# Performance work log

Measured on AMD Instinct MI355X. Metric: run time of the kernel, lower is better.

Reference implementation:

```python
import jax, jax.numpy as jnp
import numpy as np
import math

B, S, H, NH = 2, 2048, 2048, 16
HD = H // NH
BASE = 10000.0


def _rope_tables():
    inv_freq = 1.0 / (BASE ** (np.arange(0, HD, 2, dtype=np.float32) / HD))
    t = np.arange(S, dtype=np.float32)
    freqs = np.einsum('i,j->ij', t, inv_freq)          # [S, HD/2]
    emb = np.concatenate([freqs, freqs], axis=-1)       # [S, HD]
    return jnp.asarray(np.cos(emb)), jnp.asarray(np.sin(emb))


def setup_inputs() -> dict:
    key = jax.random.key(0)
    ks = jax.random.split(key, 6)
    scale = 1.0 / math.sqrt(H)
    cos, sin = _rope_tables()
    causal = np.triu(np.full((S, S), -1e9, dtype=np.float32), k=1)
    attn_bias = jnp.broadcast_to(jnp.asarray(causal)[None, None], (B, 1, S, S))
    return {
        'hidden_states': jax.random.normal(ks[0], (B, S, H), jnp.float32),
        'masks': jnp.zeros((B, S, S), jnp.float32),
        'attn_bias': attn_bias,
        'cos': cos,
        'sin': sin,
        'wq': jax.random.normal(ks[1], (H, H), jnp.float32) * scale,
        'wk': jax.random.normal(ks[2], (H, H), jnp.float32) * scale,
        'wv': jax.random.normal(ks[3], (H, H), jnp.float32) * scale,
        'wo': jax.random.normal(ks[4], (H, H), jnp.float32) * scale,
        'position_ids': jnp.broadcast_to(jnp.arange(S, dtype=jnp.int64)[None], (B, S)),
    }


def _rotate_half(x):
    x1, x2 = x[..., : x.shape[-1] // 2], x[..., x.shape[-1] // 2:]
    return jnp.concatenate([-x2, x1], axis=-1)


def reference(hidden_states, masks, attn_bias, cos, sin, wq, wk, wv, wo, position_ids):
    b, s, h = hidden_states.shape
    nh, hd = NH, HD
    # QKV projections (torch Linear: x @ W.T), split heads -> [b, nh, s, hd]
    def proj(w):
        return (hidden_states @ w.T).reshape(b, s, nh, hd).transpose(0, 2, 1, 3)
    q, k, v = proj(wq), proj(wk), proj(wv)
    # RoPE
    cos_p = cos[position_ids][:, None]  # [b, 1, s, hd]
    sin_p = sin[position_ids][:, None]
    q = q * cos_p + _rotate_half(q) * sin_p
    k = k * cos_p + _rotate_half(k) * sin_p
    # attention scores with additive masks (mx_attn branch, fp math)
    att = jnp.einsum('bhqd,bhkd->bhqk', q / math.sqrt(hd), k)
    att = att + attn_bias + masks[:, None]
    att = jax.nn.softmax(att, axis=-1)
    out = jnp.einsum('bhqk,bhkd->bhqd', att, v)
    out = out.transpose(0, 2, 1, 3).reshape(b, s, h)
    return out @ wo.T
```

## Files before the change

### kernel.cpp

```cpp
#include <hip/hip_runtime.h>
#include <stdint.h>

#define B_  2
#define S_  2048
#define H_  2048
#define NH_ 16
#define HD_ 128

typedef __bf16 v8bf __attribute__((ext_vector_type(8)));
typedef float  v4f  __attribute__((ext_vector_type(4)));

__device__ __forceinline__ float b2f(unsigned short u) {
  union { unsigned int i; float f; } x; x.i = ((unsigned int)u) << 16; return x.f;
}
__device__ __forceinline__ unsigned short f2b(float f) {
  union { float f; unsigned int i; } x; x.f = f;
  unsigned int r = x.i + 0x7FFFu + ((x.i >> 16) & 1u);
  return (unsigned short)(r >> 16);
}

__device__ __forceinline__ void async16(const void* g, void* l) {
  __builtin_amdgcn_global_load_lds(
      (const __attribute__((address_space(1))) void*)g,
      (__attribute__((address_space(3))) void*)l, 16, 0, 0);
}

__global__ __launch_bounds__(256) void cvt_all(const float* __restrict__ hid,
                                               const float* __restrict__ wq,
                                               const float* __restrict__ wk,
                                               const float* __restrict__ wv,
                                               const float* __restrict__ wo,
                                               unsigned short* __restrict__ Xb,
                                               unsigned short* __restrict__ Wqb,
                                               unsigned short* __restrict__ Wkb,
                                               unsigned short* __restrict__ Wvb,
                                               unsigned short* __restrict__ Wob) {
  int bid = blockIdx.x;
  const float* src;
  unsigned short* dst;
  int rel;
  if (bid < 8192)       { src = hid; dst = Xb;  rel = bid; }
  else if (bid < 12288) { src = wq;  dst = Wqb; rel = bid - 8192; }
  else if (bid < 16384) { src = wk;  dst = Wkb; rel = bid - 12288; }
  else if (bid < 20480) { src = wv;  dst = Wvb; rel = bid - 16384; }
  else                  { src = wo;  dst = Wob; rel = bid - 20480; }
  int i = rel * 256 + threadIdx.x;
  float4 f = *(const float4*)(src + (size_t)i * 4);
  ushort4 u;
  u.x = f2b(f.x); u.y = f2b(f.y); u.z = f2b(f.z); u.w = f2b(f.w);
  *(ushort4*)(dst + (size_t)i * 4) = u;
}

__device__ __forceinline__ void gemm_tile_nt(const unsigned short* __restrict__ A,
                                             const unsigned short* __restrict__ Bm,
                                             int m0, int n0, int Kdim,
                                             unsigned short* As, unsigned short* Bs,
                                             v4f (&acc)[2][8]) {
  const int tid = threadIdx.x;
  const int lane = tid & 63, w = tid >> 6;
  const int lr = lane & 15, lg = lane >> 4;
  const int wm = w * 32;

  for (int k0 = 0; k0 < Kdim; k0 += 32) {
    __syncthreads();
#pragma unroll
    for (int i = 0; i < 2; ++i) {
      const int cbase = i * 256 + w * 64;
      const int cc = cbase + lane;
      const int row = cc >> 2, col = (cc & 3) << 3;
      async16(A  + (size_t)(m0 + row) * Kdim + k0 + col, (char*)As + (size_t)cbase * 16);
      async16(Bm + (size_t)(n0 + row) * Kdim + k0 + col, (char*)Bs + (size_t)cbase * 16);
    }
    __syncthreads();
    v8bf a[2], bb[8];
#pragma unroll
    for (int i = 0; i < 2; i++) a[i]  = *(const v8bf*)(As + (wm + i * 16 + lr) * 32 + lg * 8);
#pragma unroll
    for (int i = 0; i < 8; i++) bb[i] = *(const v8bf*)(Bs + (i * 16 + lr) * 32 + lg * 8);
#pragma unroll
    for (int mi = 0; mi < 2; mi++)
#pragma unroll
      for (int ni = 0; ni < 8; ni++)
        acc[mi][ni] = __builtin_amdgcn_mfma_f32_16x16x32_bf16(a[mi], bb[ni], acc[mi][ni], 0, 0, 0);
  }
}

__global__ __launch_bounds__(256, 2) void gemm_qkv(const unsigned short* __restrict__ X,
                                                   const unsigned short* __restrict__ Wq,
                                                   const unsigned short* __restrict__ Wk,
                                                   const unsigned short* __restrict__ Wv,
                                                   const float* __restrict__ cosT,
                                                   const float* __restrict__ sinT,
                                                   unsigned short* __restrict__ Qo,
                                                   unsigned short* __restrict__ Ko,
                                                   unsigned short* __restrict__ Vt) {
  __shared__ unsigned short As[128 * 32], Bs[128 * 32];
  const int m0 = blockIdx.x * 128;
  const int ny = blockIdx.y;
  const int sel = ny >> 4;
  const int h = ny & 15;
  const unsigned short* Bm = (sel == 0) ? Wq : (sel == 1 ? Wk : Wv);
  const int n0 = h * 128;

  v4f acc[2][8];
#pragma unroll
  for (int i = 0; i < 2; i++)
#pragma unroll
    for (int j = 0; j < 8; j++) { v4f z = {0.f, 0.f, 0.f, 0.f}; acc[i][j] = z; }

  gemm_tile_nt(X, Bm, m0, n0, H_, As, Bs, acc);

  const int lane = threadIdx.x & 63, w = threadIdx.x >> 6;
  const int lr = lane & 15, lg = lane >> 4;
  const int rbase = m0 + w * 32;

  if (sel < 2) {
    unsigned short* Out = (sel == 0) ? Qo : Ko;
    const float sc = (sel == 0) ? (float)(0.08838834764831845 * 1.4426950408889634) : 1.0f;
#pragma unroll
    for (int mi = 0; mi < 2; mi++)
#pragma unroll
      for (int ni = 0; ni < 4; ni++)
#pragma unroll
        for (int r = 0; r < 4; r++) {
          int row = rbase + mi * 16 + lg * 4 + r;
          int s = row & 2047;
          int d = ni * 16 + lr;
          float c  = cosT[(size_t)s * HD_ + d];
          float sn = sinT[(size_t)s * HD_ + d];
          float x1 = acc[mi][ni][r], x2 = acc[mi][ni + 4][r];
          Out[(size_t)row * H_ + n0 + d]      = f2b((x1 * c - x2 * sn) * sc);
          Out[(size_t)row * H_ + n0 + d + 64] = f2b((x2 * c + x1 * sn) * sc);
        }
  } else {
#pragma unroll
    for (int mi = 0; mi < 2; mi++)
#pragma unroll
      for (int ni = 0; ni < 8; ni++) {
        int row0 = rbase + mi * 16 + lg * 4;
        int b = row0 >> 11, s0 = row0 & 2047;
        int d = ni * 16 + lr;
        ushort4 u;
        u.x = f2b(acc[mi][ni][0]); u.y = f2b(acc[mi][ni][1]);
        u.z = f2b(acc[mi][ni][2]); u.w = f2b(acc[mi][ni][3]);
        *(ushort4*)(Vt + ((size_t)((b * NH_ + h) * HD_) + d) * S_ + s0) = u;
      }
  }
}

__global__ __launch_bounds__(256, 2) void gemm_out(const unsigned short* __restrict__ A,
                                                   const unsigned short* __restrict__ Wo,
                                                   float* __restrict__ Out) {
  __shared__ unsigned short As[128 * 32], Bs[128 * 32];
  const int m0 = blockIdx.x * 128;
  const int n0 = blockIdx.y * 128;

  v4f acc[2][8];
#pragma unroll
  for (int i = 0; i < 2; i++)
#pragma unroll
    for (int j = 0; j < 8; j++) { v4f z = {0.f, 0.f, 0.f, 0.f}; acc[i][j] = z; }

  gemm_tile_nt(A, Wo, m0, n0, H_, As, Bs, acc);

  const int lane = threadIdx.x & 63, w = threadIdx.x >> 6;
  const int lr = lane & 15, lg = lane >> 4;
#pragma unroll
  for (int mi = 0; mi < 2; mi++)
#pragma unroll
    for (int ni = 0; ni < 8; ni++)
#pragma unroll
      for (int r = 0; r < 4; r++)
        Out[(size_t)(m0 + w * 32 + mi * 16 + lg * 4 + r) * H_ + n0 + ni * 16 + lr] =
            acc[mi][ni][r];
}

#define KT_ 64

__global__ __launch_bounds__(512, 2) void attn_kernel(const unsigned short* __restrict__ Qb,
                                                      const unsigned short* __restrict__ Kb,
                                                      const unsigned short* __restrict__ Vt,
                                                      unsigned short* __restrict__ Ob) {
  __shared__ __align__(16) char smem[90112];
  unsigned short* Ps = (unsigned short*)(smem + 71680);

  const int tid = threadIdx.x, lane = tid & 63, w = tid >> 6;
  const int lr = lane & 15, lg = lane >> 4;
  const int qp = blockIdx.x, h = blockIdx.y, b = blockIdx.z;

  const int wtile = (w < 4) ? qp : (15 - qp);
  const int wrow = wtile * 128 + (w & 3) * 32;
  const int nkt = (16 - qp) * 2;

  auto stage = [&](int kt, char* Kd) {
    const int k0 = kt * KT_;
    char* Vd = Kd + 17408;
#pragma unroll
    for (int i = 0; i < 3; ++i) {
      int cbase = i * 512 + w * 64;
      if (cbase < 1088) {
        int cc = cbase + lane;
        int row = cc / 17, pos = cc % 17;
        int p2 = (pos == 16) ? 0 : pos;
        async16(Kb + (size_t)(b * S_ + k0 + row) * H_ + h * HD_ + p2 * 8,
                Kd + (size_t)cbase * 16);
      }
    }
#pragma unroll
    for (int i = 0; i < 3; ++i) {
      int cbase = i * 512 + w * 64;
      if (cbase < 1152) {
        int cc = cbase + lane;
        int row = cc / 9, pos = cc % 9;
        int p2 = (pos == 8) ? 0 : pos;
        async16(Vt + ((size_t)((b * NH_ + h) * HD_ + row)) * S_ + k0 + p2 * 8,
                Vd + (size_t)cbase * 16);
      }
    }
  };

  v8bf qf[2][4];
#pragma unroll
  for (int mt = 0; mt < 2; mt++)
#pragma unroll
    for (int ks = 0; ks < 4; ks++)
      qf[mt][ks] = *(const v8bf*)(Qb + (size_t)(b * S_ + wrow + mt * 16 + lr) * H_ +
                                  h * HD_ + ks * 32 + lg * 8);

  v4f o[2][8];
#pragma unroll
  for (int mt = 0; mt < 2; mt++)
#pragma unroll
    for (int nt = 0; nt < 8; nt++) { v4f z = {0.f, 0.f, 0.f, 0.f}; o[mt][nt] = z; }
  float mst[2][4], lst[2][4];
#pragma unroll
  for (int mt = 0; mt < 2; mt++)
#pragma unroll
    for (int r = 0; r < 4; r++) { mst[mt][r] = -1e30f; lst[mt][r] = 0.f; }

  stage(0, smem);
  __syncthreads();

  int cur = 0;
  for (int kt = 0; kt < nkt; kt++) {
    char* curb = smem + cur * 35840;
    if (kt + 1 < nkt) stage(kt + 1, smem + (cur ^ 1) * 35840);

    unsigned short* Ks = (unsigned short*)curb;
    unsigned short* Vs = (unsigned short*)(curb + 17408);
    const int k0 = kt * KT_;

    if (k0 <= wrow + 31) {
      v4f sacc[2][4];
#pragma unroll
      for (int mt = 0; mt < 2; mt++)
#pragma unroll
        for (int nt = 0; nt < 4; nt++) { v4f z = {0.f, 0.f, 0.f, 0.f}; sacc[mt][nt] = z; }
#pragma unroll
      for (int nt = 0; nt < 4; nt++) {
        v8bf kf[4];
#pragma unroll
        for (int ks = 0; ks < 4; ks++)
          kf[ks] = *(const v8bf*)(Ks + (nt * 16 + lr) * 136 + ks * 32 + lg * 8);
#pragma unroll
        for (int mt = 0; mt < 2; mt++)
#pragma unroll
          for (int ks = 0; ks < 4; ks++)
            sacc[mt][nt] =
                __builtin_amdgcn_mfma_f32_16x16x32_bf16(qf[mt][ks], kf[ks], sacc[mt][nt], 0, 0, 0);
      }
      if (k0 + KT_ - 1 > wrow) {
#pragma unroll
        for (int mt = 0; mt < 2; mt++)
#pragma unroll
          for (int nt = 0; nt < 4; nt++)
#pragma unroll
            for (int r = 0; r < 4; r++) {
              int key = k0 + nt * 16 + lr;
              int query = wrow + mt * 16 + lg * 4 + r;
              if (key > query) sacc[mt][nt][r] = -1e30f;
            }
      }
#pragma unroll
      for (int mt = 0; mt < 2; mt++) {
        float rmax[4], alpha[4], rsum[4];
#pragma unroll
        for (int r = 0; r < 4; r++) {
          float v = fmaxf(fmaxf(sacc[mt][0][r], sacc[mt][1][r]),
                          fmaxf(sacc[mt][2][r], sacc[mt][3][r]));
#pragma unroll
          for (int off = 8; off >= 1; off >>= 1) v = fmaxf(v, __shfl_xor(v, off, 64));
          rmax[r] = v;
        }
#pragma unroll
        for (int r = 0; r < 4; r++) {
          float mnew = fmaxf(mst[mt][r], rmax[r]);
          alpha[r] = exp2f(mst[mt][r] - mnew);
          mst[mt][r] = mnew;
          rsum[r] = 0.f;
        }
#pragma unroll
        for (int nt = 0; nt < 4; nt++)
#pragma unroll
          for (int r = 0; r < 4; r++) {
            float p = exp2f(sacc[mt][nt][r] - mst[mt][r]);
            sacc[mt][nt][r] = p;
            rsum[r] += p;
          }
#pragma unroll
        for (int r = 0; r < 4; r++) {
#pragma unroll
          for (int off = 8; off >= 1; off >>= 1) rsum[r] += __shfl_xor(rsum[r], off, 64);
          lst[mt][r] = lst[mt][r] * alpha[r] + rsum[r];
        }
#pragma unroll
        for (int nt = 0; nt < 8; nt++)
#pragma unroll
          for (int r = 0; r < 4; r++) o[mt][nt][r] *= alpha[r];
      }
      v8bf bv[8][2];
#pragma unroll
      for (int nt = 0; nt < 8; nt++)
#pragma unroll
        for (int ks = 0; ks < 2; ks++)
          bv[nt][ks] = *(const v8bf*)(Vs + (nt * 16 + lr) * 72 + ks * 32 + lg * 8);
#pragma unroll
      for (int mt = 0; mt < 2; mt++) {
#pragma unroll
        for (int nt = 0; nt < 4; nt++)
#pragma unroll
          for (int r = 0; r < 4; r++) {
            union { float f; unsigned u; } pu; pu.f = sacc[mt][nt][r];
            Ps[w * 1152 + (lg * 4 + r) * 72 + nt * 16 + lr] =
                (unsigned short)(pu.u >> 16);
          }
        asm volatile("" ::: "memory");
        v8bf af[2];
#pragma unroll
        for (int ks = 0; ks < 2; ks++)
          af[ks] = *(const v8bf*)(Ps + w * 1152 + lr * 72 + ks * 32 + lg * 8);
#pragma unroll
        for (int nt = 0; nt < 8; nt++)
#pragma unroll
          for (int ks = 0; ks < 2; ks++)
            o[mt][nt] = __builtin_amdgcn_mfma_f32_16x16x32_bf16(af[ks], bv[nt][ks], o[mt][nt], 0, 0, 0);
        asm volatile("" ::: "memory");
      }
    }
    __syncthreads();
    cur ^= 1;
  }
#pragma unroll
  for (int mt = 0; mt < 2; mt++) {
    float inv[4];
#pragma unroll
    for (int r = 0; r < 4; r++) inv[r] = 1.f / lst[mt][r];
#pragma unroll
    for (int nt = 0; nt < 8; nt++)
#pragma unroll
      for (int r = 0; r < 4; r++) {
        int row = wrow + mt * 16 + lg * 4 + r;
        int col = h * HD_ + nt * 16 + lr;
        Ob[(size_t)(b * S_ + row) * H_ + col] = f2b(o[mt][nt][r] * inv[r]);
      }
  }
}

extern "C" void kernel_launch(void* const* d_in, const int* in_sizes, int n_in,
                              void* d_out, int out_size, void* d_ws, size_t ws_size,
                              hipStream_t stream) {
  const float* hidden = (const float*)d_in[0];
  const float* cosT = (const float*)d_in[3];
  const float* sinT = (const float*)d_in[4];
  const float* wq = (const float*)d_in[5];
  const float* wk = (const float*)d_in[6];
  const float* wv = (const float*)d_in[7];
  const float* wo = (const float*)d_in[8];
  float* out = (float*)d_out;

  char* p = (char*)d_ws;
  const size_t SZ_X = (size_t)4096 * 2048 * 2;
  const size_t SZ_W = (size_t)2048 * 2048 * 2;
  unsigned short* Xb  = (unsigned short*)p; p += SZ_X;
  unsigned short* Wqb = (unsigned short*)p; p += SZ_W;
  unsigned short* Wkb = (unsigned short*)p; p += SZ_W;
  unsigned short* Wvb = (unsigned short*)p; p += SZ_W;
  unsigned short* Wob = (unsigned short*)p; p += SZ_W;
  unsigned short* Qb  = (unsigned short*)p; p += SZ_X;
  unsigned short* Kb  = (unsigned short*)p; p += SZ_X;
  unsigned short* Vt  = (unsigned short*)p; p += SZ_X;
  unsigned short* Ob  = (unsigned short*)p; p += SZ_X;

  cvt_all<<<24576, 256, 0, stream>>>(hidden, wq, wk, wv, wo, Xb, Wqb, Wkb, Wvb, Wob);
  gemm_qkv<<<dim3(32, 48), 256, 0, stream>>>(Xb, Wqb, Wkb, Wvb, cosT, sinT, Qb, Kb, Vt);
  attn_kernel<<<dim3(8, 16, 2), 512, 0, stream>>>(Qb, Kb, Vt, Ob);
  gemm_out<<<dim3(32, 16), 256, 0, stream>>>(Ob, Wob, out);
}
```

Measured before the change: 448.6 us.

## Pipeline GEMMs with 4-stage async LDS ring, retile QKV, swizzle attention LDS

The QKV GEMM becomes a 512-thread kernel with 256x256 tiles for Q/K, followed by a second pass for V using 256x128 tiles, all fed by a 4-deep global_load_lds ring with explicit vmcnt waits and a raised MFMA priority. The output GEMM gets the same multi-stage ring instead of a load-sync-compute loop. The attention kernel drops padded LDS rows in favour of XOR-swizzled layouts, reassigns each wave 16 rows from a long and a short causal tile so MFMA work is skipped for masked short rows, and replaces shuffle reductions with ds_swizzle. Together these aim to hide global load latency and cut LDS bank conflicts and wasted causal work, at the cost of much larger LDS use, fewer QKV blocks, and hand-tuned waitcnt values that must stay consistent with the number of loads issued.

Result: faster. 426.9 us (-4.8%).

```diff
diff --git a/kernel.cpp b/kernel.cpp
--- a/kernel.cpp
+++ b/kernel.cpp
@@ -23,6 +23,21 @@
   __builtin_amdgcn_global_load_lds(
       (const __attribute__((address_space(1))) void*)g,
       (__attribute__((address_space(3))) void*)l, 16, 0, 0);
+}
+
+__device__ __forceinline__ float swz_max16(float v) {
+  v = fmaxf(v, __int_as_float(__builtin_amdgcn_ds_swizzle(__float_as_int(v), 0x201F)));
+  v = fmaxf(v, __int_as_float(__builtin_amdgcn_ds_swizzle(__float_as_int(v), 0x101F)));
+  v = fmaxf(v, __int_as_float(__builtin_amdgcn_ds_swizzle(__float_as_int(v), 0x081F)));
+  v = fmaxf(v, __int_as_float(__builtin_amdgcn_ds_swizzle(__float_as_int(v), 0x041F)));
+  return v;
+}
+__device__ __forceinline__ float swz_sum16(float v) {
+  v += __int_as_float(__builtin_amdgcn_ds_swizzle(__float_as_int(v), 0x201F));
+  v += __int_as_float(__builtin_amdgcn_ds_swizzle(__float_as_int(v), 0x101F));
+  v += __int_as_float(__builtin_amdgcn_ds_swizzle(__float_as_int(v), 0x081F));
+  v += __int_as_float(__builtin_amdgcn_ds_swizzle(__float_as_int(v), 0x041F));
+  return v;
 }
 
 __global__ __launch_bounds__(256) void cvt_all(const float* __restrict__ hid,
@@ -51,41 +66,7 @@
   *(ushort4*)(dst + (size_t)i * 4) = u;
 }
 
-__device__ __forceinline__ void gemm_tile_nt(const unsigned short* __restrict__ A,
-                                             const unsigned short* __restrict__ Bm,
-                                             int m0, int n0, int Kdim,
-                                             unsigned short* As, unsigned short* Bs,
-                                             v4f (&acc)[2][8]) {
-  const int tid = threadIdx.x;
-  const int lane = tid & 63, w = tid >> 6;
-  const int lr = lane & 15, lg = lane >> 4;
-  const int wm = w * 32;
-
-  for (int k0 = 0; k0 < Kdim; k0 += 32) {
-    __syncthreads();
-#pragma unroll
-    for (int i = 0; i < 2; ++i) {
-      const int cbase = i * 256 + w * 64;
-      const int cc = cbase + lane;
-      const int row = cc >> 2, col = (cc & 3) << 3;
-      async16(A  + (size_t)(m0 + row) * Kdim + k0 + col, (char*)As + (size_t)cbase * 16);
-      async16(Bm + (size_t)(n0 + row) * Kdim + k0 + col, (char*)Bs + (size_t)cbase * 16);
-    }
-    __syncthreads();
-    v8bf a[2], bb[8];
-#pragma unroll
-    for (int i = 0; i < 2; i++) a[i]  = *(const v8bf*)(As + (wm + i * 16 + lr) * 32 + lg * 8);
-#pragma unroll
-    for (int i = 0; i < 8; i++) bb[i] = *(const v8bf*)(Bs + (i * 16 + lr) * 32 + lg * 8);
-#pragma unroll
-    for (int mi = 0; mi < 2; mi++)
-#pragma unroll
-      for (int ni = 0; ni < 8; ni++)
-        acc[mi][ni] = __builtin_amdgcn_mfma_f32_16x16x32_bf16(a[mi], bb[ni], acc[mi][ni], 0, 0, 0);
-  }
-}
-
-__global__ __launch_bounds__(256, 2) void gemm_qkv(const unsigned short* __restrict__ X,
+__global__ __launch_bounds__(512, 2) void gemm_qkv(const unsigned short* __restrict__ X,
                                                    const unsigned short* __restrict__ Wq,
                                                    const unsigned short* __restrict__ Wk,
                                                    const unsigned short* __restrict__ Wv,
@@ -94,52 +75,152 @@
                                                    unsigned short* __restrict__ Qo,
                                                    unsigned short* __restrict__ Ko,
                                                    unsigned short* __restrict__ Vt) {
-  __shared__ unsigned short As[128 * 32], Bs[128 * 32];
-  const int m0 = blockIdx.x * 128;
-  const int ny = blockIdx.y;
-  const int sel = ny >> 4;
-  const int h = ny & 15;
-  const unsigned short* Bm = (sel == 0) ? Wq : (sel == 1 ? Wk : Wv);
-  const int n0 = h * 128;
-
-  v4f acc[2][8];
-#pragma unroll
-  for (int i = 0; i < 2; i++)
-#pragma unroll
-    for (int j = 0; j < 8; j++) { v4f z = {0.f, 0.f, 0.f, 0.f}; acc[i][j] = z; }
-
-  gemm_tile_nt(X, Bm, m0, n0, H_, As, Bs, acc);
-
-  const int lane = threadIdx.x & 63, w = threadIdx.x >> 6;
+  __shared__ __align__(16) unsigned short lds[65536];
+  unsigned short* ldsA = lds;
+  unsigned short* ldsB = lds + 32768;
+
+  const int tid = threadIdx.x, lane = tid & 63, w = tid >> 6;
   const int lr = lane & 15, lg = lane >> 4;
-  const int rbase = m0 + w * 32;
-
-  if (sel < 2) {
-    unsigned short* Out = (sel == 0) ? Qo : Ko;
-    const float sc = (sel == 0) ? (float)(0.08838834764831845 * 1.4426950408889634) : 1.0f;
-#pragma unroll
-    for (int mi = 0; mi < 2; mi++)
+  const int wm = w >> 1, wn = w & 1;
+  const int m0 = blockIdx.x * 256;
+  const int by = blockIdx.y;
+
+  {
+    const int nq = by & 7;
+    const int n0 = nq * 256;
+    const unsigned short* Bw = (by < 8) ? Wq : Wk;
+
+    v4f acc[4][8];
+#pragma unroll
+    for (int i = 0; i < 4; i++)
+#pragma unroll
+      for (int j = 0; j < 8; j++) { v4f z = {0.f, 0.f, 0.f, 0.f}; acc[i][j] = z; }
+
+    auto stage1 = [&](int ss) {
+      unsigned short* Ad = ldsA + (ss & 3) * 8192;
+      unsigned short* Bd = ldsB + (ss & 3) * 8192;
+      const int k0 = ss * 32;
+#pragma unroll
+      for (int i = 0; i < 2; ++i) {
+        int cbase = i * 512 + w * 64;
+        int cc = cbase + lane;
+        int row = cc >> 2, pos = cc & 3;
+        async16(X  + (size_t)(m0 + row) * H_ + k0 + pos * 8, (char*)Ad + (size_t)cbase * 16);
+        async16(Bw + (size_t)(n0 + row) * H_ + k0 + pos * 8, (char*)Bd + (size_t)cbase * 16);
+      }
+    };
+
+    stage1(0); stage1(1); stage1(2);
+
+#define QKV_SLICE(S, VMSTR) do {                                               \
+    asm volatile("s_waitcnt vmcnt(" VMSTR ") lgkmcnt(0)" ::: "memory");        \
+    __builtin_amdgcn_s_barrier();                                              \
+    if ((S) + 3 < 64) stage1((S) + 3);                                         \
+    const unsigned short* As_ = ldsA + ((S) & 3) * 8192;                       \
+    const unsigned short* Bs_ = ldsB + ((S) & 3) * 8192;                       \
+    v8bf bf[8], af[4];                                                         \
+    _Pragma("unroll") for (int ni = 0; ni < 8; ni++)                           \
+      bf[ni] = *(const v8bf*)(Bs_ + (wn * 128 + ni * 16 + lr) * 32 + lg * 8);  \
+    _Pragma("unroll") for (int mi = 0; mi < 4; mi++)                           \
+      af[mi] = *(const v8bf*)(As_ + (wm * 64 + mi * 16 + lr) * 32 + lg * 8);   \
+    __builtin_amdgcn_s_setprio(1);                                             \
+    _Pragma("unroll") for (int mi = 0; mi < 4; mi++)                           \
+      _Pragma("unroll") for (int ni = 0; ni < 8; ni++)                         \
+        acc[mi][ni] = __builtin_amdgcn_mfma_f32_16x16x32_bf16(af[mi], bf[ni],  \
+                                                              acc[mi][ni], 0, 0, 0); \
+    __builtin_amdgcn_s_setprio(0);                                             \
+  } while (0)
+
+    for (int s = 0; s < 62; ++s) QKV_SLICE(s, "8");
+    QKV_SLICE(62, "4");
+    QKV_SLICE(63, "0");
+#undef QKV_SLICE
+
+    const int h = nq * 2 + wn;
+    const int rb0 = m0 + wm * 64;
+    unsigned short* Out = (by < 8) ? Qo : Ko;
+    const float sc = (by < 8) ? (float)(0.08838834764831845 * 1.4426950408889634) : 1.0f;
+#pragma unroll
+    for (int mi = 0; mi < 4; mi++)
 #pragma unroll
       for (int ni = 0; ni < 4; ni++)
 #pragma unroll
         for (int r = 0; r < 4; r++) {
-          int row = rbase + mi * 16 + lg * 4 + r;
+          int row = rb0 + mi * 16 + lg * 4 + r;
           int s = row & 2047;
           int d = ni * 16 + lr;
           float c  = cosT[(size_t)s * HD_ + d];
           float sn = sinT[(size_t)s * HD_ + d];
           float x1 = acc[mi][ni][r], x2 = acc[mi][ni + 4][r];
-          Out[(size_t)row * H_ + n0 + d]      = f2b((x1 * c - x2 * sn) * sc);
-          Out[(size_t)row * H_ + n0 + d + 64] = f2b((x2 * c + x1 * sn) * sc);
+          Out[(size_t)row * H_ + h * HD_ + d]      = f2b((x1 * c - x2 * sn) * sc);
+          Out[(size_t)row * H_ + h * HD_ + d + 64] = f2b((x2 * c + x1 * sn) * sc);
         }
-  } else {
-#pragma unroll
-    for (int mi = 0; mi < 2; mi++)
-#pragma unroll
-      for (int ni = 0; ni < 8; ni++) {
-        int row0 = rbase + mi * 16 + lg * 4;
+  }
+
+  __syncthreads();
+
+  {
+    const int n0v = by * 128;
+
+    v4f acc[4][4];
+#pragma unroll
+    for (int i = 0; i < 4; i++)
+#pragma unroll
+      for (int j = 0; j < 4; j++) { v4f z = {0.f, 0.f, 0.f, 0.f}; acc[i][j] = z; }
+
+    auto stage2 = [&](int ss) {
+      unsigned short* Ad = ldsA + (ss & 3) * 8192;
+      unsigned short* Bd = ldsB + (ss & 3) * 4096;
+      const int k0 = ss * 32;
+#pragma unroll
+      for (int i = 0; i < 2; ++i) {
+        int cbase = i * 512 + w * 64;
+        int cc = cbase + lane;
+        int row = cc >> 2, pos = cc & 3;
+        async16(X + (size_t)(m0 + row) * H_ + k0 + pos * 8, (char*)Ad + (size_t)cbase * 16);
+      }
+      {
+        int cbase = w * 64;
+        int cc = cbase + lane;
+        int row = cc >> 2, pos = cc & 3;
+        async16(Wv + (size_t)(n0v + row) * H_ + k0 + pos * 8, (char*)Bd + (size_t)cbase * 16);
+      }
+    };
+
+    stage2(0); stage2(1); stage2(2);
+
+#define V_SLICE(S, VMSTR) do {                                                 \
+    asm volatile("s_waitcnt vmcnt(" VMSTR ") lgkmcnt(0)" ::: "memory");        \
+    __builtin_amdgcn_s_barrier();                                              \
+    if ((S) + 3 < 64) stage2((S) + 3);                                         \
+    const unsigned short* As_ = ldsA + ((S) & 3) * 8192;                       \
+    const unsigned short* Bs_ = ldsB + ((S) & 3) * 4096;                       \
+    v8bf bf[4], af[4];                                                         \
+    _Pragma("unroll") for (int ni = 0; ni < 4; ni++)                           \
+      bf[ni] = *(const v8bf*)(Bs_ + (wn * 64 + ni * 16 + lr) * 32 + lg * 8);   \
+    _Pragma("unroll") for (int mi = 0; mi < 4; mi++)                           \
+      af[mi] = *(const v8bf*)(As_ + (wm * 64 + mi * 16 + lr) * 32 + lg * 8);   \
+    __builtin_amdgcn_s_setprio(1);                                             \
+    _Pragma("unroll") for (int mi = 0; mi < 4; mi++)                           \
+      _Pragma("unroll") for (int ni = 0; ni < 4; ni++)                         \
+        acc[mi][ni] = __builtin_amdgcn_mfma_f32_16x16x32_bf16(af[mi], bf[ni],  \
+                                                              acc[mi][ni], 0, 0, 0); \
+    __builtin_amdgcn_s_setprio(0);                                             \
+  } while (0)
+
+    for (int s = 0; s < 62; ++s) V_SLICE(s, "6");
+    V_SLICE(62, "3");
+    V_SLICE(63, "0");
+#undef V_SLICE
+
+    const int h = by;
+#pragma unroll
+    for (int mi = 0; mi < 4; mi++)
+#pragma unroll
+      for (int ni = 0; ni < 4; ni++) {
+        int row0 = m0 + wm * 64 + mi * 16 + lg * 4;
         int b = row0 >> 11, s0 = row0 & 2047;
-        int d = ni * 16 + lr;
+        int d = wn * 64 + ni * 16 + lr;
         ushort4 u;
         u.x = f2b(acc[mi][ni][0]); u.y = f2b(acc[mi][ni][1]);
         u.z = f2b(acc[mi][ni][2]); u.w = f2b(acc[mi][ni][3]);
@@ -151,7 +232,12 @@
 __global__ __launch_bounds__(256, 2) void gemm_out(const unsigned short* __restrict__ A,
                                                    const unsigned short* __restrict__ Wo,
                                                    float* __restrict__ Out) {
-  __shared__ unsigned short As[128 * 32], Bs[128 * 32];
+  __shared__ __align__(16) unsigned short lds[32768];
+  unsigned short* ldsA = lds;
+  unsigned short* ldsB = lds + 16384;
+
+  const int tid = threadIdx.x, lane = tid & 63, w = tid >> 6;
+  const int lr = lane & 15, lg = lane >> 4;
   const int m0 = blockIdx.x * 128;
   const int n0 = blockIdx.y * 128;
 
@@ -161,10 +247,46 @@
 #pragma unroll
     for (int j = 0; j < 8; j++) { v4f z = {0.f, 0.f, 0.f, 0.f}; acc[i][j] = z; }
 
-  gemm_tile_nt(A, Wo, m0, n0, H_, As, Bs, acc);
-
-  const int lane = threadIdx.x & 63, w = threadIdx.x >> 6;
-  const int lr = lane & 15, lg = lane >> 4;
+  auto stage = [&](int ss) {
+    unsigned short* Ad = ldsA + (ss & 3) * 4096;
+    unsigned short* Bd = ldsB + (ss & 3) * 4096;
+    const int k0 = ss * 32;
+#pragma unroll
+    for (int i = 0; i < 2; ++i) {
+      int cbase = i * 256 + w * 64;
+      int cc = cbase + lane;
+      int row = cc >> 2, pos = cc & 3;
+      async16(A  + (size_t)(m0 + row) * H_ + k0 + pos * 8, (char*)Ad + (size_t)cbase * 16);
+      async16(Wo + (size_t)(n0 + row) * H_ + k0 + pos * 8, (char*)Bd + (size_t)cbase * 16);
+    }
+  };
+
+  stage(0); stage(1); stage(2);
+
+#define O_SLICE(S, VMSTR) do {                                                 \
+    asm volatile("s_waitcnt vmcnt(" VMSTR ") lgkmcnt(0)" ::: "memory");        \
+    __builtin_amdgcn_s_barrier();                                              \
+    if ((S) + 3 < 64) stage((S) + 3);                                          \
+    const unsigned short* As_ = ldsA + ((S) & 3) * 4096;                       \
+    const unsigned short* Bs_ = ldsB + ((S) & 3) * 4096;                       \
+    v8bf bf[8], af[2];                                                         \
+    _Pragma("unroll") for (int ni = 0; ni < 8; ni++)                           \
+      bf[ni] = *(const v8bf*)(Bs_ + (ni * 16 + lr) * 32 + lg * 8);             \
+    _Pragma("unroll") for (int mi = 0; mi < 2; mi++)                           \
+      af[mi] = *(const v8bf*)(As_ + (w * 32 + mi * 16 + lr) * 32 + lg * 8);    \
+    __builtin_amdgcn_s_setprio(1);                                             \
+    _Pragma("unroll") for (int mi = 0; mi < 2; mi++)                           \
+      _Pragma("unroll") for (int ni = 0; ni < 8; ni++)                         \
+        acc[mi][ni] = __builtin_amdgcn_mfma_f32_16x16x32_bf16(af[mi], bf[ni],  \
+                                                              acc[mi][ni], 0, 0, 0); \
+    __builtin_amdgcn_s_setprio(0);                                             \
+  } while (0)
+
+  for (int s = 0; s < 62; ++s) O_SLICE(s, "8");
+  O_SLICE(62, "4");
+  O_SLICE(63, "0");
+#undef O_SLICE
+
 #pragma unroll
   for (int mi = 0; mi < 2; mi++)
 #pragma unroll
@@ -181,51 +303,47 @@
                                                       const unsigned short* __restrict__ Kb,
                                                       const unsigned short* __restrict__ Vt,
                                                       unsigned short* __restrict__ Ob) {
-  __shared__ __align__(16) char smem[90112];
-  unsigned short* Ps = (unsigned short*)(smem + 71680);
+  __shared__ __align__(16) char smem[83968];
+  unsigned short* Ps = (unsigned short*)(smem + 65536);
 
   const int tid = threadIdx.x, lane = tid & 63, w = tid >> 6;
   const int lr = lane & 15, lg = lane >> 4;
   const int qp = blockIdx.x, h = blockIdx.y, b = blockIdx.z;
 
-  const int wtile = (w < 4) ? qp : (15 - qp);
-  const int wrow = wtile * 128 + (w & 3) * 32;
+  const int lrow = (15 - qp) * 128 + w * 16;
+  const int srow = qp * 128 + w * 16;
   const int nkt = (16 - qp) * 2;
+  const int xsw = (lr & 7) << 3;
 
   auto stage = [&](int kt, char* Kd) {
     const int k0 = kt * KT_;
-    char* Vd = Kd + 17408;
-#pragma unroll
-    for (int i = 0; i < 3; ++i) {
+    char* Vd = Kd + 16384;
+#pragma unroll
+    for (int i = 0; i < 2; ++i) {
       int cbase = i * 512 + w * 64;
-      if (cbase < 1088) {
-        int cc = cbase + lane;
-        int row = cc / 17, pos = cc % 17;
-        int p2 = (pos == 16) ? 0 : pos;
-        async16(Kb + (size_t)(b * S_ + k0 + row) * H_ + h * HD_ + p2 * 8,
-                Kd + (size_t)cbase * 16);
-      }
+      int cc = cbase + lane;
+      int row = cc >> 4, pos = cc & 15;
+      async16(Kb + (size_t)(b * S_ + k0 + row) * H_ + h * HD_ + ((pos ^ (row & 7)) << 3),
+              Kd + (size_t)cbase * 16);
     }
 #pragma unroll
-    for (int i = 0; i < 3; ++i) {
+    for (int i = 0; i < 2; ++i) {
       int cbase = i * 512 + w * 64;
-      if (cbase < 1152) {
-        int cc = cbase + lane;
-        int row = cc / 9, pos = cc % 9;
-        int p2 = (pos == 8) ? 0 : pos;
-        async16(Vt + ((size_t)((b * NH_ + h) * HD_ + row)) * S_ + k0 + p2 * 8,
-                Vd + (size_t)cbase * 16);
-      }
+      int cc = cbase + lane;
+      int row = cc >> 3, pos = cc & 7;
+      async16(Vt + ((size_t)((b * NH_ + h) * HD_ + row)) * S_ + k0 + ((pos ^ (row & 7)) << 3),
+              Vd + (size_t)cbase * 16);
     }
   };
 
   v8bf qf[2][4];
 #pragma unroll
-  for (int mt = 0; mt < 2; mt++)
-#pragma unroll
-    for (int ks = 0; ks < 4; ks++)
-      qf[mt][ks] = *(const v8bf*)(Qb + (size_t)(b * S_ + wrow + mt * 16 + lr) * H_ +
-                                  h * HD_ + ks * 32 + lg * 8);
+  for (int ks = 0; ks < 4; ks++) {
+    qf[0][ks] = *(const v8bf*)(Qb + (size_t)(b * S_ + lrow + lr) * H_ +
+                               h * HD_ + ks * 32 + lg * 8);
+    qf[1][ks] = *(const v8bf*)(Qb + (size_t)(b * S_ + srow + lr) * H_ +
+                               h * HD_ + ks * 32 + lg * 8);
+  }
 
   v4f o[2][8];
 #pragma unroll
@@ -243,14 +361,15 @@
 
   int cur = 0;
   for (int kt = 0; kt < nkt; kt++) {
-    char* curb = smem + cur * 35840;
-    if (kt + 1 < nkt) stage(kt + 1, smem + (cur ^ 1) * 35840);
+    char* curb = smem + cur * 32768;
+    if (kt + 1 < nkt) stage(kt + 1, smem + (cur ^ 1) * 32768);
 
     unsigned short* Ks = (unsigned short*)curb;
-    unsigned short* Vs = (unsigned short*)(curb + 17408);
+    unsigned short* Vs = (unsigned short*)(curb + 16384);
     const int k0 = kt * KT_;
 
-    if (k0 <= wrow + 31) {
+    if (k0 <= lrow + 15) {
+      const bool act1 = (k0 <= srow + 15);
       v4f sacc[2][4];
 #pragma unroll
       for (int mt = 0; mt < 2; mt++)
@@ -261,40 +380,43 @@
         v8bf kf[4];
 #pragma unroll
         for (int ks = 0; ks < 4; ks++)
-          kf[ks] = *(const v8bf*)(Ks + (nt * 16 + lr) * 136 + ks * 32 + lg * 8);
-#pragma unroll
-        for (int mt = 0; mt < 2; mt++)
+          kf[ks] = *(const v8bf*)(Ks + (nt * 16 + lr) * 128 + ((ks * 32 + lg * 8) ^ xsw));
+#pragma unroll
+        for (int ks = 0; ks < 4; ks++)
+          sacc[0][nt] = __builtin_amdgcn_mfma_f32_16x16x32_bf16(qf[0][ks], kf[ks], sacc[0][nt], 0, 0, 0);
+        if (act1)
 #pragma unroll
           for (int ks = 0; ks < 4; ks++)
-            sacc[mt][nt] =
-                __builtin_amdgcn_mfma_f32_16x16x32_bf16(qf[mt][ks], kf[ks], sacc[mt][nt], 0, 0, 0);
-      }
-      if (k0 + KT_ - 1 > wrow) {
-#pragma unroll
-        for (int mt = 0; mt < 2; mt++)
-#pragma unroll
-          for (int nt = 0; nt < 4; nt++)
-#pragma unroll
-            for (int r = 0; r < 4; r++) {
-              int key = k0 + nt * 16 + lr;
-              int query = wrow + mt * 16 + lg * 4 + r;
-              if (key > query) sacc[mt][nt][r] = -1e30f;
-            }
+            sacc[1][nt] = __builtin_amdgcn_mfma_f32_16x16x32_bf16(qf[1][ks], kf[ks], sacc[1][nt], 0, 0, 0);
+      }
+      if (k0 + 63 > lrow) {
+#pragma unroll
+        for (int nt = 0; nt < 4; nt++)
+#pragma unroll
+          for (int r = 0; r < 4; r++) {
+            int key = k0 + nt * 16 + lr;
+            if (key > lrow + lg * 4 + r) sacc[0][nt][r] = -1e30f;
+          }
+      }
+      if (act1 && k0 + 63 > srow) {
+#pragma unroll
+        for (int nt = 0; nt < 4; nt++)
+#pragma unroll
+          for (int r = 0; r < 4; r++) {
+            int key = k0 + nt * 16 + lr;
+            if (key > srow + lg * 4 + r) sacc[1][nt][r] = -1e30f;
+          }
       }
 #pragma unroll
       for (int mt = 0; mt < 2; mt++) {
-        float rmax[4], alpha[4], rsum[4];
+        if (mt == 1 && !act1) continue;
+        float alpha[4], rsum[4];
 #pragma unroll
         for (int r = 0; r < 4; r++) {
           float v = fmaxf(fmaxf(sacc[mt][0][r], sacc[mt][1][r]),
                           fmaxf(sacc[mt][2][r], sacc[mt][3][r]));
-#pragma unroll
-          for (int off = 8; off >= 1; off >>= 1) v = fmaxf(v, __shfl_xor(v, off, 64));
-          rmax[r] = v;
-        }
-#pragma unroll
-        for (int r = 0; r < 4; r++) {
-          float mnew = fmaxf(mst[mt][r], rmax[r]);
+          v = swz_max16(v);
+          float mnew = fmaxf(mst[mt][r], v);
           alpha[r] = exp2f(mst[mt][r] - mnew);
           mst[mt][r] = mnew;
           rsum[r] = 0.f;
@@ -309,8 +431,7 @@
           }
 #pragma unroll
         for (int r = 0; r < 4; r++) {
-#pragma unroll
-          for (int off = 8; off >= 1; off >>= 1) rsum[r] += __shfl_xor(rsum[r], off, 64);
+          rsum[r] = swz_sum16(rsum[r]);
           lst[mt][r] = lst[mt][r] * alpha[r] + rsum[r];
         }
 #pragma unroll
@@ -323,9 +444,10 @@
       for (int nt = 0; nt < 8; nt++)
 #pragma unroll
         for (int ks = 0; ks < 2; ks++)
-          bv[nt][ks] = *(const v8bf*)(Vs + (nt * 16 + lr) * 72 + ks * 32 + lg * 8);
+          bv[nt][ks] = *(const v8bf*)(Vs + (nt * 16 + lr) * 64 + ((ks * 32 + lg * 8) ^ xsw));
 #pragma unroll
       for (int mt = 0; mt < 2; mt++) {
+        if (mt == 1 && !act1) continue;
 #pragma unroll
         for (int nt = 0; nt < 4; nt++)
 #pragma unroll
@@ -352,6 +474,7 @@
   }
 #pragma unroll
   for (int mt = 0; mt < 2; mt++) {
+    const int rbase = (mt == 0) ? lrow : srow;
     float inv[4];
 #pragma unroll
     for (int r = 0; r < 4; r++) inv[r] = 1.f / lst[mt][r];
@@ -359,7 +482,7 @@
     for (int nt = 0; nt < 8; nt++)
 #pragma unroll
       for (int r = 0; r < 4; r++) {
-        int row = wrow + mt * 16 + lg * 4 + r;
+        int row = rbase + lg * 4 + r;
         int col = h * HD_ + nt * 16 + lr;
         Ob[(size_t)(b * S_ + row) * H_ + col] = f2b(o[mt][nt][r] * inv[r]);
       }
@@ -392,7 +515,7 @@
   unsigned short* Ob  = (unsigned short*)p; p += SZ_X;
 
   cvt_all<<<24576, 256, 0, stream>>>(hidden, wq, wk, wv, wo, Xb, Wqb, Wkb, Wvb, Wob);
-  gemm_qkv<<<dim3(32, 48), 256, 0, stream>>>(Xb, Wqb, Wkb, Wvb, cosT, sinT, Qb, Kb, Vt);
+  gemm_qkv<<<dim3(16, 16), 512, 0, stream>>>(Xb, Wqb, Wkb, Wvb, cosT, sinT, Qb, Kb, Vt);
   attn_kernel<<<dim3(8, 16, 2), 512, 0, stream>>>(Qb, Kb, Vt, Ob);
   gemm_out<<<dim3(32, 16), 256, 0, stream>>>(Ob, Wob, out);
 }
```
